# Optimization experiments

Hardware: AMD Instinct MI355X
Metric: run time of the kernel (lower is better)

The kernel has to match this reference:

```python
import jax, jax.numpy as jnp
import numpy as np
from jax import lax

TEMPERATURE = 34.0
PAD = 1

def setup_inputs() -> dict:
    key = jax.random.key(0)
    ks = jax.random.split(key, 6)
    B, C, H, W = 16, 256, 64, 64
    K, O, kk, hidden = 4, 256, 3, int(256 * 0.25) + 1
    return {
        "x": jax.random.normal(ks[0], (B, C, H, W), jnp.float32),
        "w_fc1": jax.random.normal(ks[1], (hidden, C), jnp.float32) * 0.05,
        "w_fc2": jax.random.normal(ks[2], (K, hidden), jnp.float32) * 0.05,
        "b_fc2": jax.random.normal(ks[3], (K,), jnp.float32) * 0.05,
        "weight": jax.random.normal(ks[4], (K, O, C, kk, kk), jnp.float32) * 0.05,
        "bias": jax.random.normal(ks[5], (K, O), jnp.float32) * 0.05,
    }

def reference(x, w_fc1, w_fc2, b_fc2, weight, bias):
    # attention2d: global avg pool -> 1x1 conv -> relu -> 1x1 conv -> softmax(logits/T)
    pooled = jnp.mean(x, axis=(2, 3))                       # [B, C]
    h = jax.nn.relu(pooled @ w_fc1.T)                       # [B, hidden]
    logits = h @ w_fc2.T + b_fc2                            # [B, K]
    att = jax.nn.softmax(logits / TEMPERATURE, axis=1)      # [B, K]

    K = weight.shape[0]
    # per-sample aggregated kernels/bias
    agg_w = jnp.einsum('bk,koihw->boihw', att, weight)      # [B, O, C, k, k]
    agg_b = att @ bias                                      # [B, O]

    def conv_one(xi, wi):
        # xi: [C, H, W], wi: [O, C, k, k]
        return lax.conv_general_dilated(
            xi[None], wi, window_strides=(1, 1),
            padding=[(PAD, PAD), (PAD, PAD)],
            dimension_numbers=('NCHW', 'OIHW', 'NCHW'))[0]

    out = jax.vmap(conv_one)(x, agg_w)                      # [B, O, H, W]
    return out + agg_b[:, :, None, None]
```

## Files before the change

### kernel.cpp

```cpp
#include <hip/hip_runtime.h>
#include <math.h>

constexpr int B   = 16;
constexpr int C   = 256;
constexpr int H   = 64;
constexpr int W   = 64;
constexpr int K   = 4;
constexpr int O   = 256;
constexpr int HID = 65;
constexpr float TEMP = 34.0f;

typedef __bf16 bf16x8 __attribute__((ext_vector_type(8)));
typedef float  f32x16 __attribute__((ext_vector_type(16)));
typedef unsigned short ushort_t;

__device__ inline ushort_t f2bf(float f) {
    union { float f; unsigned u; } v; v.f = f;
    unsigned u = v.u;
    u += 0x7FFF + ((u >> 16) & 1);
    return (ushort_t)(u >> 16);
}

__device__ inline void gl2lds16(const void* g, void* l) {
    __builtin_amdgcn_global_load_lds(
        (const __attribute__((address_space(1))) unsigned int*)g,
        (__attribute__((address_space(3))) unsigned int*)l, 16, 0, 0);
}

__global__ void tp_kernel(const float* __restrict__ x,
                          ushort_t* __restrict__ xT,
                          float* __restrict__ pooled) {
    const int ci = blockIdx.x, yg = blockIdx.y, b = blockIdx.z;
    const int tid = threadIdx.x;
    const int cc = tid >> 4;
    const int yy = tid & 15;
    const int y  = yg * 16 + yy;
    const int c  = ci * 16 + cc;

    __shared__ ushort_t t_lds[16 * 1040];
    __shared__ float pool_l[16];
    if (tid < 16) pool_l[tid] = 0.f;
    __syncthreads();

    const float4* src = (const float4*)(x + (((size_t)b * C + c) * H + y) * W);
    float s = 0.f;
    #pragma unroll
    for (int i = 0; i < 16; ++i) {
        float4 v = src[i];
        s += (v.x + v.y) + (v.z + v.w);
        ushort_t* d = &t_lds[yy * 1040 + (4 * i) * 16 + cc];
        d[0]  = f2bf(v.x);
        d[16] = f2bf(v.y);
        d[32] = f2bf(v.z);
        d[48] = f2bf(v.w);
    }
    atomicAdd(&pool_l[cc], s);
    __syncthreads();
    if (tid < 16)
        atomicAdd(&pooled[b * C + ci * 16 + tid], pool_l[tid] * (1.0f / (H * W)));

    const int w    = tid >> 6;
    const int lane = tid & 63;
    const int col  = lane >> 1;
    const int half = lane & 1;
    #pragma unroll
    for (int q = 0; q < 4; ++q) {
        const int y2 = w * 4 + q;
        ushort_t* gbase = xT + ((((size_t)b * 16 + ci) * 64 + (yg * 16 + y2)) * 64) * 16;
        #pragma unroll
        for (int sseg = 0; sseg < 2; ++sseg) {
            uint4 v = *(const uint4*)&t_lds[y2 * 1040 + (sseg * 32 + col) * 16 + half * 8];
            *(uint4*)(gbase + sseg * 512 + lane * 8) = v;
        }
    }
}

__global__ void attention_kernel(const float* __restrict__ pooled,
                                 const float* __restrict__ w_fc1,
                                 const float* __restrict__ w_fc2,
                                 const float* __restrict__ b_fc2,
                                 float* __restrict__ att) {
    const int b = blockIdx.x;
    const int tid = threadIdx.x;
    __shared__ float pool_s[C];
    __shared__ float h_s[HID];
    __shared__ float logit_s[K];

    for (int i = tid; i < C; i += blockDim.x) pool_s[i] = pooled[b * C + i];
    __syncthreads();
    for (int j = tid; j < HID; j += blockDim.x) {
        const float* wr = w_fc1 + (size_t)j * C;
        float s = 0.f;
        #pragma unroll 4
        for (int c = 0; c < C; ++c) s += pool_s[c] * wr[c];
        h_s[j] = fmaxf(s, 0.f);
    }
    __syncthreads();
    if (tid < K) {
        const float* wr = w_fc2 + (size_t)tid * HID;
        float s = b_fc2[tid];
        for (int j = 0; j < HID; ++j) s += h_s[j] * wr[j];
        logit_s[tid] = s * (1.0f / TEMP);
    }
    __syncthreads();
    if (tid == 0) {
        float m = fmaxf(fmaxf(logit_s[0], logit_s[1]), fmaxf(logit_s[2], logit_s[3]));
        float e0 = expf(logit_s[0] - m), e1 = expf(logit_s[1] - m);
        float e2 = expf(logit_s[2] - m), e3 = expf(logit_s[3] - m);
        float inv = 1.0f / (e0 + e1 + e2 + e3);
        att[b * K + 0] = e0 * inv; att[b * K + 1] = e1 * inv;
        att[b * K + 2] = e2 * inv; att[b * K + 3] = e3 * inv;
    }
}

__global__ void wagg_kernel(const float* __restrict__ weight,
                            const float* __restrict__ att,
                            ushort_t* __restrict__ wagg_sw) {
    const int o = blockIdx.x;
    const int tid = threadIdx.x;
    const int oct = tid >> 3;
    const int bg  = tid & 7;

    __shared__ float att_s[B * K];
    if (tid < B * K) att_s[tid] = att[tid];
    __syncthreads();

    const int mi   = o >> 5;
    const int lm   = o & 31;
    const int ci   = oct >> 1;
    const int half = oct & 1;
    const int lane = half * 32 + lm;

    for (int t = 0; t < 9; ++t) {
        float w0[8], w1[8], w2[8], w3[8];
        #pragma unroll
        for (int j = 0; j < 8; ++j) {
            const size_t cidx = (size_t)(oct * 8 + j) * 9 + t;
            w0[j] = weight[((size_t)(0 * O + o) * C) * 9 + cidx];
            w1[j] = weight[((size_t)(1 * O + o) * C) * 9 + cidx];
            w2[j] = weight[((size_t)(2 * O + o) * C) * 9 + cidx];
            w3[j] = weight[((size_t)(3 * O + o) * C) * 9 + cidx];
        }
        #pragma unroll
        for (int bb = 0; bb < 2; ++bb) {
            const int b = bg * 2 + bb;
            const float a0 = att_s[b * K + 0], a1 = att_s[b * K + 1];
            const float a2 = att_s[b * K + 2], a3 = att_s[b * K + 3];
            union { ushort_t u[8]; uint4 v; } pk;
            #pragma unroll
            for (int j = 0; j < 8; ++j)
                pk.u[j] = f2bf(a0 * w0[j] + a1 * w1[j] + a2 * w2[j] + a3 * w3[j]);
            size_t idx = ((((size_t)b * 16 + ci) * 9 + t) * 8 + mi) * 512 + lane * 8;
            *(uint4*)&wagg_sw[idx] = pk.v;
        }
    }
}

__global__ __launch_bounds__(256, 2)
void conv_mfma_kernel(const ushort_t* __restrict__ xT,
                      const ushort_t* __restrict__ wagg_sw,
                      const float* __restrict__ bias,
                      const float* __restrict__ att,
                      float* __restrict__ out) {
    const int b  = blockIdx.x;
    const int yt = blockIdx.y;
    const int oz = blockIdx.z;
    const int y0 = yt * 4;

    const int tid  = threadIdx.x;
    const int lane = tid & 63;
    const int wid  = tid >> 6;
    const int n16  = lane & 31;
    const int khalf = lane >> 5;

    __shared__ __align__(16) ushort_t A_lds[9 * 4 * 512];
    __shared__ __align__(16) ushort_t x_lds[6 * 66 * 16];

    for (int i = tid; i < 6 * 66 * 16; i += 256) x_lds[i] = 0;

    f32x16 acc[4][2];
    #pragma unroll
    for (int a = 0; a < 4; ++a)
        #pragma unroll
        for (int ni = 0; ni < 2; ++ni)
            acc[a][ni] = (f32x16)(0.f);

    for (int ci = 0; ci < 16; ++ci) {
        __syncthreads();

        for (int i = wid; i < 36; i += 4) {
            const int t = i >> 2, a = i & 3;
            const ushort_t* g = wagg_sw
                + ((((size_t)b * 16 + ci) * 9 + t) * 8 + (oz * 4 + a)) * 512 + lane * 8;
            gl2lds16(g, &A_lds[(t * 4 + a) * 512]);
        }
        for (int r = wid; r < 6; r += 4) {
            const int y = y0 - 1 + r;
            if ((unsigned)y < (unsigned)H) {
                const ushort_t* gr = xT + ((((size_t)b * 16 + ci) * 64 + y) * 64) * 16;
                #pragma unroll
                for (int h = 0; h < 2; ++h)
                    gl2lds16(gr + h * 512 + lane * 8,
                             &x_lds[r * (66 * 16) + 16 + h * 512]);
            }
        }

        __syncthreads();

        #pragma unroll
        for (int dy = 0; dy < 3; ++dy) {
            const int r = wid + dy;
            #pragma unroll
            for (int dx = 0; dx < 3; ++dx) {
                const int t = dy * 3 + dx;
                bf16x8 bf[2];
                #pragma unroll
                for (int ni = 0; ni < 2; ++ni)
                    bf[ni] = *(const bf16x8*)&x_lds[r * (66 * 16)
                              + (ni * 32 + n16 + dx) * 16 + khalf * 8];
                #pragma unroll
                for (int a = 0; a < 4; ++a) {
                    bf16x8 af = *(const bf16x8*)&A_lds[(t * 4 + a) * 512 + lane * 8];
                    acc[a][0] = __builtin_amdgcn_mfma_f32_32x32x16_bf16(af, bf[0], acc[a][0], 0, 0, 0);
                    acc[a][1] = __builtin_amdgcn_mfma_f32_32x32x16_bf16(af, bf[1], acc[a][1], 0, 0, 0);
                }
            }
        }
    }

    __syncthreads();
    float* aggb = (float*)A_lds;
    if (tid < 128) {
        const int o = oz * 128 + tid;
        aggb[tid] = att[b * K + 0] * bias[0 * O + o] + att[b * K + 1] * bias[1 * O + o]
                  + att[b * K + 2] * bias[2 * O + o] + att[b * K + 3] * bias[3 * O + o];
    }
    __syncthreads();

    const int y = y0 + wid;
    #pragma unroll
    for (int a = 0; a < 4; ++a) {
        #pragma unroll
        for (int ni = 0; ni < 2; ++ni) {
            #pragma unroll
            for (int reg = 0; reg < 16; ++reg) {
                const int row = (reg & 3) + 8 * (reg >> 2) + 4 * khalf;
                const int ol  = a * 32 + row;
                out[(((size_t)b * O + oz * 128 + ol) * H + y) * W + ni * 32 + n16]
                    = acc[a][ni][reg] + aggb[ol];
            }
        }
    }
}

__global__ void pool_kernel(const float* __restrict__ x, float* __restrict__ pooled) {
    const int bc = blockIdx.x;
    const float4* p4 = (const float4*)(x + (size_t)bc * (H * W));
    const int tid = threadIdx.x;
    float s = 0.f;
    #pragma unroll
    for (int i = 0; i < (H * W / 4) / 256; ++i) {
        float4 v = p4[tid + i * 256];
        s += (v.x + v.y) + (v.z + v.w);
    }
    #pragma unroll
    for (int off = 32; off > 0; off >>= 1) s += __shfl_down(s, off, 64);
    __shared__ float red[4];
    if ((tid & 63) == 0) red[tid >> 6] = s;
    __syncthreads();
    if (tid == 0) pooled[bc] = ((red[0] + red[1]) + (red[2] + red[3])) * (1.0f / (H * W));
}

constexpr int TILE_H = 32;
constexpr int TILE_W = 64;
constexpr int CCF = 4, OT = 8, PX = 8;
constexpr int XS_STRIDE = TILE_W + 3;

__global__ __launch_bounds__(256, 2)
void conv_kernel(const float* __restrict__ x, const float* __restrict__ weight,
                 const float* __restrict__ bias, const float* __restrict__ att,
                 float* __restrict__ out) {
    const int tile_y = blockIdx.x, o0 = blockIdx.y * OT, b = blockIdx.z;
    const int tid = threadIdx.x, tx = tid & 7, ty = tid >> 3, ty0 = tile_y * TILE_H;
    __shared__ __align__(16) float xs[CCF][TILE_H + 2][XS_STRIDE];
    __shared__ __align__(16) float ws_s[OT][CCF][12];
    const float a0 = att[b * K + 0], a1 = att[b * K + 1];
    const float a2 = att[b * K + 2], a3 = att[b * K + 3];
    float acc[OT][PX];
    #pragma unroll
    for (int o = 0; o < OT; ++o)
        #pragma unroll
        for (int p = 0; p < PX; ++p) acc[o][p] = 0.f;
    const float* xb = x + (size_t)b * C * H * W;
    constexpr int X_ELEMS = CCF * (TILE_H + 2) * (TILE_W + 2);
    constexpr int W_ELEMS = OT * CCF * 9;
    for (int c0 = 0; c0 < C; c0 += CCF) {
        __syncthreads();
        for (int idx = tid; idx < X_ELEMS; idx += 256) {
            int cc = idx / ((TILE_H + 2) * (TILE_W + 2));
            int rem = idx - cc * ((TILE_H + 2) * (TILE_W + 2));
            int r = rem / (TILE_W + 2), col = rem - r * (TILE_W + 2);
            int gy = ty0 - 1 + r, gx = col - 1;
            float v = 0.f;
            if ((unsigned)gy < (unsigned)H && (unsigned)gx < (unsigned)W)
                v = xb[((size_t)(c0 + cc) * H + gy) * W + gx];
            xs[cc][r][col] = v;
        }
        for (int idx = tid; idx < W_ELEMS; idx += 256) {
            int o = idx / (CCF * 9), rem = idx - o * (CCF * 9);
            int cc = rem / 9, tap = rem - cc * 9;
            size_t base = ((size_t)(o0 + o) * C + (c0 + cc)) * 9 + tap;
            ws_s[o][cc][tap] = a0 * weight[base] + a1 * weight[(size_t)1 * O * C * 9 + base]
                             + a2 * weight[(size_t)2 * O * C * 9 + base]
                             + a3 * weight[(size_t)3 * O * C * 9 + base];
        }
        __syncthreads();
        #pragma unroll
        for (int cc = 0; cc < CCF; ++cc) {
            float xv[3][10];
            #pragma unroll
            for (int dy = 0; dy < 3; ++dy)
                #pragma unroll
                for (int j = 0; j < 10; ++j) xv[dy][j] = xs[cc][ty + dy][8 * tx + j];
            #pragma unroll
            for (int o = 0; o < OT; ++o) {
                float4 w0 = *(const float4*)&ws_s[o][cc][0];
                float4 w1 = *(const float4*)&ws_s[o][cc][4];
                float w8 = ws_s[o][cc][8];
                #pragma unroll
                for (int p = 0; p < PX; ++p) {
                    float s = acc[o][p];
                    s = fmaf(xv[0][p + 0], w0.x, s); s = fmaf(xv[0][p + 1], w0.y, s);
                    s = fmaf(xv[0][p + 2], w0.z, s); s = fmaf(xv[1][p + 0], w0.w, s);
                    s = fmaf(xv[1][p + 1], w1.x, s); s = fmaf(xv[1][p + 2], w1.y, s);
                    s = fmaf(xv[2][p + 0], w1.z, s); s = fmaf(xv[2][p + 1], w1.w, s);
                    s = fmaf(xv[2][p + 2], w8, s);
                    acc[o][p] = s;
                }
            }
        }
    }
    const int oy = ty0 + ty, ox = 8 * tx;
    #pragma unroll
    for (int o = 0; o < OT; ++o) {
        float ab = a0 * bias[0 * O + o0 + o] + a1 * bias[1 * O + o0 + o]
                 + a2 * bias[2 * O + o0 + o] + a3 * bias[3 * O + o0 + o];
        float4 v0 = make_float4(acc[o][0] + ab, acc[o][1] + ab, acc[o][2] + ab, acc[o][3] + ab);
        float4 v1 = make_float4(acc[o][4] + ab, acc[o][5] + ab, acc[o][6] + ab, acc[o][7] + ab);
        float* op = out + (((size_t)b * O + (o0 + o)) * H + oy) * W + ox;
        *(float4*)(op) = v0; *(float4*)(op + 4) = v1;
    }
}

extern "C" void kernel_launch(void* const* d_in, const int* in_sizes, int n_in,
                              void* d_out, int out_size, void* d_ws, size_t ws_size,
                              hipStream_t stream) {
    const float* x      = (const float*)d_in[0];
    const float* w_fc1  = (const float*)d_in[1];
    const float* w_fc2  = (const float*)d_in[2];
    const float* b_fc2  = (const float*)d_in[3];
    const float* weight = (const float*)d_in[4];
    const float* bias   = (const float*)d_in[5];
    float* out = (float*)d_out;

    float* pooled = (float*)d_ws;
    float* att    = pooled + B * C;
    ushort_t* wagg_sw = (ushort_t*)((char*)d_ws + 32 * 1024);
    const size_t wagg_bytes = (size_t)B * 16 * 9 * 8 * 512 * 2;
    ushort_t* xT = (ushort_t*)((char*)wagg_sw + wagg_bytes);
    const size_t xT_bytes = (size_t)B * 16 * 64 * 64 * 16 * 2;
    const size_t needed = 32 * 1024 + wagg_bytes + xT_bytes;

    if (ws_size >= needed) {
        hipMemsetAsync(pooled, 0, B * C * sizeof(float), stream);
        tp_kernel<<<dim3(16, 4, B), dim3(256), 0, stream>>>(x, xT, pooled);
        attention_kernel<<<dim3(B), dim3(128), 0, stream>>>(pooled, w_fc1, w_fc2, b_fc2, att);
        wagg_kernel<<<dim3(O), dim3(256), 0, stream>>>(weight, att, wagg_sw);
        conv_mfma_kernel<<<dim3(B, 16, 2), dim3(256), 0, stream>>>(xT, wagg_sw, bias, att, out);
    } else {
        pool_kernel<<<dim3(B * C), dim3(256), 0, stream>>>(x, pooled);
        attention_kernel<<<dim3(B), dim3(128), 0, stream>>>(pooled, w_fc1, w_fc2, b_fc2, att);
        conv_kernel<<<dim3(H / TILE_H, O / OT, B), dim3(256), 0, stream>>>(x, weight, bias, att, out);
    }
}
```

Before: 227.9 us.

## Pipeline conv input staging, load weights to registers, remove pooling atomics and memset

The conv kernel now double-buffers the x tile in LDS and prefetches the aggregated-weight fragments from global memory straight into registers two steps ahead, so the A-matrix LDS staging and one barrier per channel group go away. The transpose kernel reads coalesced float4 rows, reduces pooling with wave shuffles, and writes per-row-group partial sums, which removes the atomics and the memset launch. The wagg kernel stages each output channel's weights in LDS to avoid strided global reads, and attention uses float4 loads. The cost is more register pressure in the conv kernel and an uncoalesced LDS gather in the transpose stage.

```diff
diff --git a/kernel.cpp b/kernel.cpp
--- a/kernel.cpp
+++ b/kernel.cpp
@@ -29,53 +29,53 @@
 
 __global__ void tp_kernel(const float* __restrict__ x,
                           ushort_t* __restrict__ xT,
-                          float* __restrict__ pooled) {
+                          float* __restrict__ pooled_part) {
     const int ci = blockIdx.x, yg = blockIdx.y, b = blockIdx.z;
     const int tid = threadIdx.x;
-    const int cc = tid >> 4;
-    const int yy = tid & 15;
-    const int y  = yg * 16 + yy;
-    const int c  = ci * 16 + cc;
-
-    __shared__ ushort_t t_lds[16 * 1040];
-    __shared__ float pool_l[16];
-    if (tid < 16) pool_l[tid] = 0.f;
-    __syncthreads();
-
-    const float4* src = (const float4*)(x + (((size_t)b * C + c) * H + y) * W);
-    float s = 0.f;
-    #pragma unroll
-    for (int i = 0; i < 16; ++i) {
-        float4 v = src[i];
-        s += (v.x + v.y) + (v.z + v.w);
-        ushort_t* d = &t_lds[yy * 1040 + (4 * i) * 16 + cc];
-        d[0]  = f2bf(v.x);
-        d[16] = f2bf(v.y);
-        d[32] = f2bf(v.z);
-        d[48] = f2bf(v.w);
-    }
-    atomicAdd(&pool_l[cc], s);
-    __syncthreads();
+    const int wv  = tid >> 6, lane = tid & 63;
+
+    __shared__ ushort_t t_lds[16 * 1024];
+    __shared__ float pw[16][4];
+
+    const int yy = tid >> 4;
+    const int w4 = tid & 15;
+
+    #pragma unroll
+    for (int c = 0; c < 16; ++c) {
+        const float4 v = *(const float4*)(x
+            + (((size_t)b * C + ci * 16 + c) * H + yg * 16 + yy) * W + w4 * 4);
+        float s = (v.x + v.y) + (v.z + v.w);
+        union { ushort_t u[4]; uint2 p; } pk;
+        pk.u[0] = f2bf(v.x); pk.u[1] = f2bf(v.y);
+        pk.u[2] = f2bf(v.z); pk.u[3] = f2bf(v.w);
+        *(uint2*)&t_lds[c * 1024 + yy * 64 + w4 * 4] = pk.p;
+        #pragma unroll
+        for (int off = 32; off > 0; off >>= 1) s += __shfl_down(s, off, 64);
+        if (lane == 0) pw[c][wv] = s;
+    }
+    __syncthreads();
+
     if (tid < 16)
-        atomicAdd(&pooled[b * C + ci * 16 + tid], pool_l[tid] * (1.0f / (H * W)));
-
-    const int w    = tid >> 6;
-    const int lane = tid & 63;
-    const int col  = lane >> 1;
-    const int half = lane & 1;
-    #pragma unroll
-    for (int q = 0; q < 4; ++q) {
-        const int y2 = w * 4 + q;
-        ushort_t* gbase = xT + ((((size_t)b * 16 + ci) * 64 + (yg * 16 + y2)) * 64) * 16;
-        #pragma unroll
-        for (int sseg = 0; sseg < 2; ++sseg) {
-            uint4 v = *(const uint4*)&t_lds[y2 * 1040 + (sseg * 32 + col) * 16 + half * 8];
-            *(uint4*)(gbase + sseg * 512 + lane * 8) = v;
-        }
-    }
-}
-
-__global__ void attention_kernel(const float* __restrict__ pooled,
+        pooled_part[((size_t)yg * B + b) * C + ci * 16 + tid] =
+            (pw[tid][0] + pw[tid][1] + pw[tid][2] + pw[tid][3]) * (1.0f / (H * W));
+
+    #pragma unroll
+    for (int it = 0; it < 8; ++it) {
+        const int idx  = it * 256 + tid;
+        const int y    = idx >> 7;
+        const int rem  = idx & 127;
+        const int w    = rem >> 1;
+        const int half = rem & 1;
+        union { ushort_t u[8]; uint4 v; } pk;
+        #pragma unroll
+        for (int j = 0; j < 8; ++j)
+            pk.u[j] = t_lds[(half * 8 + j) * 1024 + y * 64 + w];
+        *(uint4*)(xT + (((size_t)(b * 16 + ci) * 64 + yg * 16 + y) * 1024)
+                  + w * 16 + half * 8) = pk.v;
+    }
+}
+
+__global__ void attention_kernel(const float* __restrict__ pooled_part,
                                  const float* __restrict__ w_fc1,
                                  const float* __restrict__ w_fc2,
                                  const float* __restrict__ b_fc2,
@@ -86,14 +86,23 @@
     __shared__ float h_s[HID];
     __shared__ float logit_s[K];
 
-    for (int i = tid; i < C; i += blockDim.x) pool_s[i] = pooled[b * C + i];
-    __syncthreads();
-    for (int j = tid; j < HID; j += blockDim.x) {
-        const float* wr = w_fc1 + (size_t)j * C;
+    for (int i = tid; i < C; i += 128)
+        pool_s[i] = pooled_part[((size_t)0 * B + b) * C + i]
+                  + pooled_part[((size_t)1 * B + b) * C + i]
+                  + pooled_part[((size_t)2 * B + b) * C + i]
+                  + pooled_part[((size_t)3 * B + b) * C + i];
+    __syncthreads();
+
+    if (tid < HID) {
+        const float4* wr = (const float4*)(w_fc1 + (size_t)tid * C);
         float s = 0.f;
-        #pragma unroll 4
-        for (int c = 0; c < C; ++c) s += pool_s[c] * wr[c];
-        h_s[j] = fmaxf(s, 0.f);
+        #pragma unroll 8
+        for (int c4 = 0; c4 < C / 4; ++c4) {
+            float4 wv = wr[c4];
+            const float* p = &pool_s[c4 * 4];
+            s += wv.x * p[0] + wv.y * p[1] + wv.z * p[2] + wv.w * p[3];
+        }
+        h_s[tid] = fmaxf(s, 0.f);
     }
     __syncthreads();
     if (tid < K) {
@@ -118,13 +127,21 @@
                             ushort_t* __restrict__ wagg_sw) {
     const int o = blockIdx.x;
     const int tid = threadIdx.x;
+
+    __shared__ float w_lds[4][2304];
+    __shared__ float att_s[B * K];
+
+    #pragma unroll
+    for (int k = 0; k < 4; ++k) {
+        const float4* src = (const float4*)(weight + ((size_t)(k * O + o)) * 2304);
+        for (int i = tid; i < 576; i += 256)
+            ((float4*)w_lds[k])[i] = src[i];
+    }
+    if (tid < B * K) att_s[tid] = att[tid];
+    __syncthreads();
+
     const int oct = tid >> 3;
     const int bg  = tid & 7;
-
-    __shared__ float att_s[B * K];
-    if (tid < B * K) att_s[tid] = att[tid];
-    __syncthreads();
-
     const int mi   = o >> 5;
     const int lm   = o & 31;
     const int ci   = oct >> 1;
@@ -135,22 +152,20 @@
         float w0[8], w1[8], w2[8], w3[8];
         #pragma unroll
         for (int j = 0; j < 8; ++j) {
-            const size_t cidx = (size_t)(oct * 8 + j) * 9 + t;
-            w0[j] = weight[((size_t)(0 * O + o) * C) * 9 + cidx];
-            w1[j] = weight[((size_t)(1 * O + o) * C) * 9 + cidx];
-            w2[j] = weight[((size_t)(2 * O + o) * C) * 9 + cidx];
-            w3[j] = weight[((size_t)(3 * O + o) * C) * 9 + cidx];
+            const int cidx = (oct * 8 + j) * 9 + t;
+            w0[j] = w_lds[0][cidx]; w1[j] = w_lds[1][cidx];
+            w2[j] = w_lds[2][cidx]; w3[j] = w_lds[3][cidx];
         }
         #pragma unroll
         for (int bb = 0; bb < 2; ++bb) {
-            const int b = bg * 2 + bb;
-            const float a0 = att_s[b * K + 0], a1 = att_s[b * K + 1];
-            const float a2 = att_s[b * K + 2], a3 = att_s[b * K + 3];
+            const int bs = bg * 2 + bb;
+            const float a0 = att_s[bs * K + 0], a1 = att_s[bs * K + 1];
+            const float a2 = att_s[bs * K + 2], a3 = att_s[bs * K + 3];
             union { ushort_t u[8]; uint4 v; } pk;
             #pragma unroll
             for (int j = 0; j < 8; ++j)
                 pk.u[j] = f2bf(a0 * w0[j] + a1 * w1[j] + a2 * w2[j] + a3 * w3[j]);
-            size_t idx = ((((size_t)b * 16 + ci) * 9 + t) * 8 + mi) * 512 + lane * 8;
+            size_t idx = ((((size_t)bs * 16 + ci) * 9 + t) * 8 + mi) * 512 + lane * 8;
             *(uint4*)&wagg_sw[idx] = pk.v;
         }
     }
@@ -173,10 +188,13 @@
     const int n16  = lane & 31;
     const int khalf = lane >> 5;
 
-    __shared__ __align__(16) ushort_t A_lds[9 * 4 * 512];
-    __shared__ __align__(16) ushort_t x_lds[6 * 66 * 16];
-
-    for (int i = tid; i < 6 * 66 * 16; i += 256) x_lds[i] = 0;
+    __shared__ __align__(16) ushort_t x_lds[2][6 * 66 * 16];
+
+    for (int i = tid; i < 2 * 6336; i += 256) ((ushort_t*)x_lds)[i] = 0;
+    __syncthreads();
+
+    const uint4* A_base = (const uint4*)wagg_sw
+        + ((((size_t)b * 16) * 9) * 8 + (size_t)oz * 4) * 64 + lane;
 
     f32x16 acc[4][2];
     #pragma unroll
@@ -185,51 +203,62 @@
         for (int ni = 0; ni < 2; ++ni)
             acc[a][ni] = (f32x16)(0.f);
 
-    for (int ci = 0; ci < 16; ++ci) {
-        __syncthreads();
-
-        for (int i = wid; i < 36; i += 4) {
-            const int t = i >> 2, a = i & 3;
-            const ushort_t* g = wagg_sw
-                + ((((size_t)b * 16 + ci) * 9 + t) * 8 + (oz * 4 + a)) * 512 + lane * 8;
-            gl2lds16(g, &A_lds[(t * 4 + a) * 512]);
-        }
-        for (int r = wid; r < 6; r += 4) {
+    auto stage_x = [&](int ci, int bufp) {
+        for (int i = wid; i < 12; i += 4) {
+            const int r = i >> 1, hh = i & 1;
             const int y = y0 - 1 + r;
             if ((unsigned)y < (unsigned)H) {
-                const ushort_t* gr = xT + ((((size_t)b * 16 + ci) * 64 + y) * 64) * 16;
-                #pragma unroll
-                for (int h = 0; h < 2; ++h)
-                    gl2lds16(gr + h * 512 + lane * 8,
-                             &x_lds[r * (66 * 16) + 16 + h * 512]);
+                const ushort_t* g = xT + (((size_t)(b * 16 + ci) * 64 + y) * 1024)
+                                  + hh * 512 + lane * 8;
+                gl2lds16(g, &x_lds[bufp][r * 1056 + 16 + hh * 512]);
             }
         }
-
+    };
+
+    union AFrag { uint4 u[4]; bf16x8 h[4]; };
+    AFrag aslot[2];
+    auto aload = [&](int slot, int s) {
+        const uint4* g = A_base + (size_t)s * 8 * 64;
+        #pragma unroll
+        for (int a = 0; a < 4; ++a) aslot[slot].u[a] = g[a * 64];
+    };
+
+    stage_x(0, 0);
+    aload(0, 0);
+    aload(1, 1);
+    __syncthreads();
+
+    for (int ci = 0; ci < 16; ++ci) {
+        if (ci < 15) stage_x(ci + 1, (ci + 1) & 1);
+        const int bufp = ci & 1;
+        #pragma unroll
+        for (int t = 0; t < 9; ++t) {
+            const int s = ci * 9 + t;
+            const int slot = s & 1;
+            const int dy = t / 3, dx = t % 3;
+            const int r = wid + dy;
+
+            bf16x8 bfv[2];
+            #pragma unroll
+            for (int ni = 0; ni < 2; ++ni)
+                bfv[ni] = *(const bf16x8*)&x_lds[bufp][r * 1056
+                           + (ni * 32 + n16 + dx) * 16 + khalf * 8];
+            bf16x8 afv[4];
+            #pragma unroll
+            for (int a = 0; a < 4; ++a) afv[a] = aslot[slot].h[a];
+
+            if (s + 2 < 144) aload(slot, s + 2);
+
+            #pragma unroll
+            for (int a = 0; a < 4; ++a) {
+                acc[a][0] = __builtin_amdgcn_mfma_f32_32x32x16_bf16(afv[a], bfv[0], acc[a][0], 0, 0, 0);
+                acc[a][1] = __builtin_amdgcn_mfma_f32_32x32x16_bf16(afv[a], bfv[1], acc[a][1], 0, 0, 0);
+            }
+        }
         __syncthreads();
-
-        #pragma unroll
-        for (int dy = 0; dy < 3; ++dy) {
-            const int r = wid + dy;
-            #pragma unroll
-            for (int dx = 0; dx < 3; ++dx) {
-                const int t = dy * 3 + dx;
-                bf16x8 bf[2];
-                #pragma unroll
-                for (int ni = 0; ni < 2; ++ni)
-                    bf[ni] = *(const bf16x8*)&x_lds[r * (66 * 16)
-                              + (ni * 32 + n16 + dx) * 16 + khalf * 8];
-                #pragma unroll
-                for (int a = 0; a < 4; ++a) {
-                    bf16x8 af = *(const bf16x8*)&A_lds[(t * 4 + a) * 512 + lane * 8];
-                    acc[a][0] = __builtin_amdgcn_mfma_f32_32x32x16_bf16(af, bf[0], acc[a][0], 0, 0, 0);
-                    acc[a][1] = __builtin_amdgcn_mfma_f32_32x32x16_bf16(af, bf[1], acc[a][1], 0, 0, 0);
-                }
-            }
-        }
-    }
-
-    __syncthreads();
-    float* aggb = (float*)A_lds;
+    }
+
+    float* aggb = (float*)x_lds;
     if (tid < 128) {
         const int o = oz * 128 + tid;
         aggb[tid] = att[b * K + 0] * bias[0 * O + o] + att[b * K + 1] * bias[1 * O + o]
@@ -269,6 +298,42 @@
     if ((tid & 63) == 0) red[tid >> 6] = s;
     __syncthreads();
     if (tid == 0) pooled[bc] = ((red[0] + red[1]) + (red[2] + red[3])) * (1.0f / (H * W));
+}
+
+__global__ void attention_fb_kernel(const float* __restrict__ pooled,
+                                    const float* __restrict__ w_fc1,
+                                    const float* __restrict__ w_fc2,
+                                    const float* __restrict__ b_fc2,
+                                    float* __restrict__ att) {
+    const int b = blockIdx.x;
+    const int tid = threadIdx.x;
+    __shared__ float pool_s[C];
+    __shared__ float h_s[HID];
+    __shared__ float logit_s[K];
+    for (int i = tid; i < C; i += 128) pool_s[i] = pooled[b * C + i];
+    __syncthreads();
+    if (tid < HID) {
+        const float* wr = w_fc1 + (size_t)tid * C;
+        float s = 0.f;
+        for (int c = 0; c < C; ++c) s += pool_s[c] * wr[c];
+        h_s[tid] = fmaxf(s, 0.f);
+    }
+    __syncthreads();
+    if (tid < K) {
+        const float* wr = w_fc2 + (size_t)tid * HID;
+        float s = b_fc2[tid];
+        for (int j = 0; j < HID; ++j) s += h_s[j] * wr[j];
+        logit_s[tid] = s * (1.0f / TEMP);
+    }
+    __syncthreads();
+    if (tid == 0) {
+        float m = fmaxf(fmaxf(logit_s[0], logit_s[1]), fmaxf(logit_s[2], logit_s[3]));
+        float e0 = expf(logit_s[0] - m), e1 = expf(logit_s[1] - m);
+        float e2 = expf(logit_s[2] - m), e3 = expf(logit_s[3] - m);
+        float inv = 1.0f / (e0 + e1 + e2 + e3);
+        att[b * K + 0] = e0 * inv; att[b * K + 1] = e1 * inv;
+        att[b * K + 2] = e2 * inv; att[b * K + 3] = e3 * inv;
+    }
 }
 
 constexpr int TILE_H = 32;
@@ -363,23 +428,23 @@
     const float* bias   = (const float*)d_in[5];
     float* out = (float*)d_out;
 
-    float* pooled = (float*)d_ws;
-    float* att    = pooled + B * C;
-    ushort_t* wagg_sw = (ushort_t*)((char*)d_ws + 32 * 1024);
+    float* pooled_part = (float*)d_ws;
+    float* att = (float*)((char*)d_ws + 64 * 1024);
+    ushort_t* wagg_sw = (ushort_t*)((char*)d_ws + 128 * 1024);
     const size_t wagg_bytes = (size_t)B * 16 * 9 * 8 * 512 * 2;
     ushort_t* xT = (ushort_t*)((char*)wagg_sw + wagg_bytes);
     const size_t xT_bytes = (size_t)B * 16 * 64 * 64 * 16 * 2;
-    const size_t needed = 32 * 1024 + wagg_bytes + xT_bytes;
+    const size_t needed = 128 * 1024 + wagg_bytes + xT_bytes;
 
     if (ws_size >= needed) {
-        hipMemsetAsync(pooled, 0, B * C * sizeof(float), stream);
-        tp_kernel<<<dim3(16, 4, B), dim3(256), 0, stream>>>(x, xT, pooled);
-        attention_kernel<<<dim3(B), dim3(128), 0, stream>>>(pooled, w_fc1, w_fc2, b_fc2, att);
+        tp_kernel<<<dim3(16, 4, B), dim3(256), 0, stream>>>(x, xT, pooled_part);
+        attention_kernel<<<dim3(B), dim3(128), 0, stream>>>(pooled_part, w_fc1, w_fc2, b_fc2, att);
         wagg_kernel<<<dim3(O), dim3(256), 0, stream>>>(weight, att, wagg_sw);
         conv_mfma_kernel<<<dim3(B, 16, 2), dim3(256), 0, stream>>>(xT, wagg_sw, bias, att, out);
     } else {
+        float* pooled = (float*)d_ws;
         pool_kernel<<<dim3(B * C), dim3(256), 0, stream>>>(x, pooled);
-        attention_kernel<<<dim3(B), dim3(128), 0, stream>>>(pooled, w_fc1, w_fc2, b_fc2, att);
+        attention_fb_kernel<<<dim3(B), dim3(128), 0, stream>>>(pooled, w_fc1, w_fc2, b_fc2, att);
         conv_kernel<<<dim3(H / TILE_H, O / OT, B), dim3(256), 0, stream>>>(x, weight, bias, att, out);
     }
 }
```

After: 468.5 us. +105.5%, slower.
